# Kernel optimization log

Measured on AMD Instinct MI355X. Metric: run time of the kernel, lower is better.

## Reference

```python
import jax, jax.numpy as jnp
import numpy as np

DIM = 1024
NUM_HEADS = 16
HEAD_DIM = DIM // NUM_HEADS
EPS = 1e-5


def setup_inputs() -> dict:
    key = jax.random.key(0)
    ks = jax.random.split(key, 8)
    B, N = 4, 2048
    s = 0.02
    return {
        "x1": jax.random.normal(ks[0], (B, N, DIM), jnp.float32),
        "x2": jax.random.normal(ks[1], (B, N, DIM), jnp.float32),
        "wq": jax.random.normal(ks[2], (DIM, DIM), jnp.float32) * s,
        "bq": jnp.zeros((DIM,), jnp.float32),
        "wkv": jax.random.normal(ks[3], (DIM, 2 * DIM), jnp.float32) * s,
        "bkv": jnp.zeros((2 * DIM,), jnp.float32),
        "gamma_q": jnp.ones((HEAD_DIM,), jnp.float32),
        "beta_q": jnp.zeros((HEAD_DIM,), jnp.float32),
        "gamma_k": jnp.ones((HEAD_DIM,), jnp.float32),
        "beta_k": jnp.zeros((HEAD_DIM,), jnp.float32),
    }


def _layernorm(x, gamma, beta):
    m = jnp.mean(x, axis=-1, keepdims=True)
    v = jnp.mean(jnp.square(x - m), axis=-1, keepdims=True)
    return (x - m) * jax.lax.rsqrt(v + EPS) * gamma + beta


def reference(x1, x2, wq, bq, wkv, bkv, gamma_q, beta_q, gamma_k, beta_k):
    B, N, C = x1.shape
    H, D = NUM_HEADS, C // NUM_HEADS
    q = x1 @ wq + bq                      # [B,N,C]
    kv = x2 @ wkv + bkv                   # [B,N,2C]
    k, v = kv[..., :C], kv[..., C:]
    # [B,N,C] -> [B,H,N,D]
    q = q.reshape(B, N, H, D).transpose(0, 2, 1, 3)
    k = k.reshape(B, N, H, D).transpose(0, 2, 1, 3)
    v = v.reshape(B, N, H, D).transpose(0, 2, 1, 3)
    q = _layernorm(q, gamma_q, beta_q)
    k = _layernorm(k, gamma_k, beta_k)
    scale = 1.0 / jnp.sqrt(jnp.asarray(D, x1.dtype))
    scores = jnp.einsum("bhnd,bhmd->bhnm", q, k) * scale
    attn = jax.nn.softmax(scores, axis=-1)
    out = jnp.einsum("bhnm,bhmd->bhnd", attn, v)  # [B,H,N,D]
    return out.transpose(0, 2, 1, 3).reshape(B, N, C)
```

## Files before the change

### kernel.cpp

```cpp
#include <hip/hip_runtime.h>
#include <hip/hip_bf16.h>

#define NHEADS 16
#define HDIM 64
#define BATCH 4
#define SEQ 2048
#define CDIM 1024
#define ROWS (BATCH * SEQ)

typedef __attribute__((ext_vector_type(8))) short short8;
typedef __attribute__((ext_vector_type(4))) float f32x4;

__device__ inline short f2bf(float f) {
    unsigned int u = __builtin_bit_cast(unsigned int, f);
    unsigned int r = (u + 0x7fffu + ((u >> 16) & 1u)) >> 16;
    return (short)r;
}

__device__ __forceinline__ void gll16(const void* g, void* l) {
    __builtin_amdgcn_global_load_lds(
        (const __attribute__((address_space(1))) unsigned int*)g,
        (__attribute__((address_space(3))) unsigned int*)l, 16, 0, 0);
}

__global__ __launch_bounds__(256) void cvt_bf16(const float* __restrict__ src,
                                                short* __restrict__ dst, int n8) {
    int i = blockIdx.x * 256 + threadIdx.x;
    if (i < n8) {
        f32x4 a = ((const f32x4*)src)[i * 2];
        f32x4 b = ((const f32x4*)src)[i * 2 + 1];
        short8 o;
        o[0] = f2bf(a[0]); o[1] = f2bf(a[1]); o[2] = f2bf(a[2]); o[3] = f2bf(a[3]);
        o[4] = f2bf(b[0]); o[5] = f2bf(b[1]); o[6] = f2bf(b[2]); o[7] = f2bf(b[3]);
        ((short8*)dst)[i] = o;
    }
}

__global__ __launch_bounds__(256) void wtrans(const float* __restrict__ W,
                                              short* __restrict__ WT, int Nw) {
    __shared__ short T[64][72];
    const int t = threadIdx.x;
    const int n0 = blockIdx.x * 64, k0 = blockIdx.y * 64;
    const int kl = t >> 2, c4 = (t & 3) * 16;
    const float* src = W + (size_t)(k0 + kl) * Nw + n0 + c4;
    short8 s0, s1;
#pragma unroll
    for (int e = 0; e < 2; e++) {
        f32x4 u = *(const f32x4*)(src + e * 4);
        s0[e * 4 + 0] = f2bf(u[0]); s0[e * 4 + 1] = f2bf(u[1]);
        s0[e * 4 + 2] = f2bf(u[2]); s0[e * 4 + 3] = f2bf(u[3]);
        f32x4 v = *(const f32x4*)(src + 8 + e * 4);
        s1[e * 4 + 0] = f2bf(v[0]); s1[e * 4 + 1] = f2bf(v[1]);
        s1[e * 4 + 2] = f2bf(v[2]); s1[e * 4 + 3] = f2bf(v[3]);
    }
    *(short8*)&T[kl][c4] = s0;
    *(short8*)&T[kl][c4 + 8] = s1;
    __syncthreads();
#pragma unroll
    for (int pass = 0; pass < 2; pass++) {
        int n = (t >> 3) + pass * 32;
        short8 o;
#pragma unroll
        for (int e = 0; e < 8; e++) o[e] = T[(t & 7) * 8 + e][n];
        *(short8*)(WT + (size_t)(n0 + n) * 1024 + k0 + (t & 7) * 8) = o;
    }
}

__global__ __launch_bounds__(256) void gemm_q_ln(
    const short* __restrict__ A,
    const short* __restrict__ BT,
    const float* __restrict__ bias,
    const float* __restrict__ gamma,
    const float* __restrict__ beta,
    short* __restrict__ Out)
{
    __shared__ short As[128][32];
    __shared__ short Bs[128][32];

    const int tid = threadIdx.x;
    const int wave = tid >> 6, lane = tid & 63;
    const int wr = wave >> 1, wc = wave & 1;
    const int quad = lane >> 4, l15 = lane & 15;
    const int rblk = blockIdx.y, cblk = blockIdx.x;

    f32x4 acc[4][4];
#pragma unroll
    for (int i = 0; i < 4; i++)
#pragma unroll
        for (int j = 0; j < 4; j++) acc[i][j] = f32x4{0.f, 0.f, 0.f, 0.f};

    const int srow = wave * 32 + (lane >> 2);
    const int scol = (lane & 3) * 8;

    for (int k0 = 0; k0 < CDIM; k0 += 32) {
        __syncthreads();
#pragma unroll
        for (int c = 0; c < 2; c++) {
            gll16(A + (size_t)(rblk * 128 + srow + c * 16) * CDIM + k0 + scol,
                  &As[srow + c * 16][scol]);
            gll16(BT + (size_t)(cblk * 128 + srow + c * 16) * CDIM + k0 + scol,
                  &Bs[srow + c * 16][scol]);
        }
        __syncthreads();

        short8 af[4], bfr[4];
#pragma unroll
        for (int i = 0; i < 4; i++)
            af[i] = *(const short8*)&As[wr * 64 + i * 16 + l15][quad * 8];
#pragma unroll
        for (int j = 0; j < 4; j++)
            bfr[j] = *(const short8*)&Bs[wc * 64 + j * 16 + l15][quad * 8];
#pragma unroll
        for (int i = 0; i < 4; i++)
#pragma unroll
            for (int j = 0; j < 4; j++)
                acc[i][j] = __builtin_amdgcn_mfma_f32_16x16x32_bf16(af[i], bfr[j], acc[i][j], 0, 0, 0);
    }

    const int col0 = cblk * 128 + wc * 64;
    const int h = col0 >> 6;
    float bv[4], gv[4], btv[4];
#pragma unroll
    for (int j = 0; j < 4; j++) {
        int d = j * 16 + l15;
        bv[j] = bias[col0 + d];
        gv[j] = gamma[d];
        btv[j] = beta[d];
    }
#pragma unroll
    for (int i = 0; i < 4; i++) {
        int rowl = rblk * 128 + wr * 64 + i * 16 + quad * 4;
#pragma unroll
        for (int reg = 0; reg < 4; reg++) {
            float x[4], s = 0.f, s2 = 0.f;
#pragma unroll
            for (int j = 0; j < 4; j++) {
                x[j] = acc[i][j][reg] + bv[j];
                s += x[j];
                s2 += x[j] * x[j];
            }
#pragma unroll
            for (int m = 1; m < 16; m <<= 1) {
                s += __shfl_xor(s, m);
                s2 += __shfl_xor(s2, m);
            }
            float mean = s * (1.f / 64.f);
            float var = s2 * (1.f / 64.f) - mean * mean;
            float rstd = rsqrtf(var + 1e-5f);
            int r = rowl + reg;
            int b = r >> 11, n = r & (SEQ - 1);
            size_t base = (((size_t)b * NHEADS + h) * SEQ + n) * 64;
#pragma unroll
            for (int j = 0; j < 4; j++) {
                float y = ((x[j] - mean) * rstd * gv[j] + btv[j]) * 0.125f;
                Out[base + j * 16 + l15] = f2bf(y);
            }
        }
    }
}

__global__ __launch_bounds__(256) void gemm_kv(
    const short* __restrict__ A,
    const short* __restrict__ BT,
    const float* __restrict__ bias,
    const float* __restrict__ gamma,
    const float* __restrict__ beta,
    short* __restrict__ KOut,
    short* __restrict__ VT)
{
    __shared__ short As[128][32];
    __shared__ short Bs[128][32];
    __shared__ short Ts[4][64][68];

    const int tid = threadIdx.x;
    const int wave = tid >> 6, lane = tid & 63;
    const int wr = wave >> 1, wc = wave & 1;
    const int quad = lane >> 4, l15 = lane & 15;
    const int rblk = blockIdx.y, cblk = blockIdx.x;

    f32x4 acc[4][4];
#pragma unroll
    for (int i = 0; i < 4; i++)
#pragma unroll
        for (int j = 0; j < 4; j++) acc[i][j] = f32x4{0.f, 0.f, 0.f, 0.f};

    const int srow = wave * 32 + (lane >> 2);
    const int scol = (lane & 3) * 8;

    for (int k0 = 0; k0 < CDIM; k0 += 32) {
        __syncthreads();
#pragma unroll
        for (int c = 0; c < 2; c++) {
            gll16(A + (size_t)(rblk * 128 + srow + c * 16) * CDIM + k0 + scol,
                  &As[srow + c * 16][scol]);
            gll16(BT + (size_t)(cblk * 128 + srow + c * 16) * CDIM + k0 + scol,
                  &Bs[srow + c * 16][scol]);
        }
        __syncthreads();

        short8 af[4], bfr[4];
#pragma unroll
        for (int i = 0; i < 4; i++)
            af[i] = *(const short8*)&As[wr * 64 + i * 16 + l15][quad * 8];
#pragma unroll
        for (int j = 0; j < 4; j++)
            bfr[j] = *(const short8*)&Bs[wc * 64 + j * 16 + l15][quad * 8];
#pragma unroll
        for (int i = 0; i < 4; i++)
#pragma unroll
            for (int j = 0; j < 4; j++)
                acc[i][j] = __builtin_amdgcn_mfma_f32_16x16x32_bf16(af[i], bfr[j], acc[i][j], 0, 0, 0);
    }

    const int col0 = cblk * 128 + wc * 64;
    const int g = col0 >> 6;
    float bv[4];
#pragma unroll
    for (int j = 0; j < 4; j++) bv[j] = bias[col0 + j * 16 + l15];

    if (g < NHEADS) {
        const int h = g;
        float gv[4], btv[4];
#pragma unroll
        for (int j = 0; j < 4; j++) {
            int d = j * 16 + l15;
            gv[j] = gamma[d];
            btv[j] = beta[d];
        }
#pragma unroll
        for (int i = 0; i < 4; i++) {
            int rowl = rblk * 128 + wr * 64 + i * 16 + quad * 4;
#pragma unroll
            for (int reg = 0; reg < 4; reg++) {
                float x[4], s = 0.f, s2 = 0.f;
#pragma unroll
                for (int j = 0; j < 4; j++) {
                    x[j] = acc[i][j][reg] + bv[j];
                    s += x[j];
                    s2 += x[j] * x[j];
                }
#pragma unroll
                for (int m = 1; m < 16; m <<= 1) {
                    s += __shfl_xor(s, m);
                    s2 += __shfl_xor(s2, m);
                }
                float mean = s * (1.f / 64.f);
                float var = s2 * (1.f / 64.f) - mean * mean;
                float rstd = rsqrtf(var + 1e-5f);
                int r = rowl + reg;
                int b = r >> 11, n = r & (SEQ - 1);
                size_t base = (((size_t)b * NHEADS + h) * SEQ + n) * 64;
#pragma unroll
                for (int j = 0; j < 4; j++) {
                    float y = (x[j] - mean) * rstd * gv[j] + btv[j];
                    KOut[base + j * 16 + l15] = f2bf(y);
                }
            }
        }
    } else {
        const int h = g - NHEADS;
#pragma unroll
        for (int i = 0; i < 4; i++)
#pragma unroll
            for (int reg = 0; reg < 4; reg++)
#pragma unroll
                for (int j = 0; j < 4; j++)
                    Ts[wave][i * 16 + quad * 4 + reg][j * 16 + l15] =
                        f2bf(acc[i][j][reg] + bv[j]);
        const int r = rblk * 128 + wr * 64 + lane;
        const int b = r >> 11, n = r & (SEQ - 1);
        const size_t vtbase = (((size_t)b * NHEADS + h) * 64) * SEQ;
#pragma unroll
        for (int e8 = 0; e8 < 8; e8++) {
            short8 v = *(const short8*)&Ts[wave][lane][e8 * 8];
#pragma unroll
            for (int e = 0; e < 8; e++)
                VT[vtbase + (size_t)(e8 * 8 + e) * SEQ + n] = v[e];
        }
    }
}

__global__ __launch_bounds__(256) void attn_fa(
    const short* __restrict__ Q,
    const short* __restrict__ Kk,
    const short* __restrict__ VT,
    float* __restrict__ Out)
{
    __shared__ short Ks[128][72];
    __shared__ short Vt[64][136];
    __shared__ short Ps[4][16][136];

    const int tid = threadIdx.x;
    const int wave = tid >> 6, lane = tid & 63;
    const int quad = lane >> 4, l15 = lane & 15;
    const int bh = blockIdx.y;
    const int b = bh >> 4, h = bh & 15;
    const int qt = blockIdx.x;
    const size_t head_base = (size_t)bh * SEQ * 64;
    const size_t vt_base = (size_t)bh * 64 * SEQ;

    const int qrow = qt * 64 + wave * 16 + l15;
    const short8 qf0 = *(const short8*)(Q + head_base + (size_t)qrow * 64 + quad * 8);
    const short8 qf1 = *(const short8*)(Q + head_base + (size_t)qrow * 64 + 32 + quad * 8);

    short8 ones;
#pragma unroll
    for (int e = 0; e < 8; e++) ones[e] = (short)0x3F80;

    f32x4 o[4];
#pragma unroll
    for (int jd = 0; jd < 4; jd++) o[jd] = f32x4{0.f, 0.f, 0.f, 0.f};
    f32x4 osum = f32x4{0.f, 0.f, 0.f, 0.f};

    const int ks_key = tid >> 1, ks_c = (tid & 1) * 4;
    const int vt_d = tid >> 2, vt_c = (tid & 3) * 4;

    for (int kt = 0; kt < 16; kt++) {
        short8 kv[4], vv[4];
        const short* kg = Kk + head_base + (size_t)(kt * 128 + ks_key) * 64 + ks_c * 8;
        const short* vg = VT + vt_base + (size_t)vt_d * SEQ + kt * 128 + vt_c * 8;
#pragma unroll
        for (int i = 0; i < 4; i++) kv[i] = ((const short8*)kg)[i];
#pragma unroll
        for (int i = 0; i < 4; i++) vv[i] = ((const short8*)vg)[i];

        __syncthreads();
#pragma unroll
        for (int i = 0; i < 4; i++) *(short8*)&Ks[ks_key][(ks_c + i) * 8] = kv[i];
#pragma unroll
        for (int i = 0; i < 4; i++) *(short8*)&Vt[vt_d][(vt_c + i) * 8] = vv[i];
        __syncthreads();

        f32x4 s[8];
#pragma unroll
        for (int jk = 0; jk < 8; jk++) {
            short8 kf0 = *(const short8*)&Ks[jk * 16 + l15][quad * 8];
            short8 kf1 = *(const short8*)&Ks[jk * 16 + l15][32 + quad * 8];
            f32x4 z = f32x4{0.f, 0.f, 0.f, 0.f};
            z = __builtin_amdgcn_mfma_f32_16x16x32_bf16(qf0, kf0, z, 0, 0, 0);
            z = __builtin_amdgcn_mfma_f32_16x16x32_bf16(qf1, kf1, z, 0, 0, 0);
            s[jk] = z;
        }

#pragma unroll
        for (int jk = 0; jk < 8; jk++)
#pragma unroll
            for (int reg = 0; reg < 4; reg++)
                Ps[wave][quad * 4 + reg][jk * 16 + l15] = f2bf(__expf(s[jk][reg]));

        short8 pf[4];
#pragma unroll
        for (int seg = 0; seg < 4; seg++)
            pf[seg] = *(const short8*)&Ps[wave][l15][seg * 32 + quad * 8];

#pragma unroll
        for (int seg = 0; seg < 4; seg++)
            osum = __builtin_amdgcn_mfma_f32_16x16x32_bf16(pf[seg], ones, osum, 0, 0, 0);
#pragma unroll
        for (int seg = 0; seg < 4; seg++)
#pragma unroll
            for (int jd = 0; jd < 4; jd++) {
                short8 vf = *(const short8*)&Vt[jd * 16 + l15][seg * 32 + quad * 8];
                o[jd] = __builtin_amdgcn_mfma_f32_16x16x32_bf16(pf[seg], vf, o[jd], 0, 0, 0);
            }
    }

#pragma unroll
    for (int reg = 0; reg < 4; reg++) {
        float inv = 1.f / osum[reg];
        int r = qt * 64 + wave * 16 + quad * 4 + reg;
        size_t base = ((size_t)b * SEQ + r) * CDIM + h * 64;
#pragma unroll
        for (int jd = 0; jd < 4; jd++)
            Out[base + jd * 16 + l15] = o[jd][reg] * inv;
    }
}

extern "C" void kernel_launch(void* const* d_in, const int* in_sizes, int n_in,
                              void* d_out, int out_size, void* d_ws, size_t ws_size,
                              hipStream_t stream) {
    const float* x1 = (const float*)d_in[0];
    const float* x2 = (const float*)d_in[1];
    const float* wq = (const float*)d_in[2];
    const float* bq = (const float*)d_in[3];
    const float* wkv = (const float*)d_in[4];
    const float* bkv = (const float*)d_in[5];
    const float* gq = (const float*)d_in[6];
    const float* btq = (const float*)d_in[7];
    const float* gk = (const float*)d_in[8];
    const float* btk = (const float*)d_in[9];
    float* out = (float*)d_out;

    short* a1 = (short*)d_ws;
    short* a2 = a1 + (size_t)ROWS * CDIM;
    short* wqT = a2 + (size_t)ROWS * CDIM;
    short* wkvT = wqT + (size_t)CDIM * CDIM;
    short* qln = wkvT + (size_t)2 * CDIM * CDIM;
    short* kln = qln + (size_t)ROWS * CDIM;
    short* vt = kln + (size_t)ROWS * CDIM;

    const int n8 = ROWS * CDIM / 8;
    cvt_bf16<<<dim3(n8 / 256), 256, 0, stream>>>(x1, a1, n8);
    cvt_bf16<<<dim3(n8 / 256), 256, 0, stream>>>(x2, a2, n8);
    wtrans<<<dim3(16, 16), 256, 0, stream>>>(wq, wqT, CDIM);
    wtrans<<<dim3(32, 16), 256, 0, stream>>>(wkv, wkvT, 2 * CDIM);

    gemm_q_ln<<<dim3(8, 64), 256, 0, stream>>>(a1, wqT, bq, gq, btq, qln);
    gemm_kv<<<dim3(16, 64), 256, 0, stream>>>(a2, wkvT, bkv, gk, btk, kln, vt);
    attn_fa<<<dim3(32, 64), 256, 0, stream>>>(qln, kln, vt, out);
}
```

Measured before the change: 357.1 us.

## Split attention keys across waves with register-direct K/V and cross-wave reduction

```diff
diff --git a/kernel.cpp b/kernel.cpp
--- a/kernel.cpp
+++ b/kernel.cpp
@@ -7,9 +7,11 @@
 #define SEQ 2048
 #define CDIM 1024
 #define ROWS (BATCH * SEQ)
+#define QSCALE (0.125f * 1.44269504088896f)
 
 typedef __attribute__((ext_vector_type(8))) short short8;
 typedef __attribute__((ext_vector_type(4))) float f32x4;
+typedef __attribute__((ext_vector_type(4))) unsigned int u32x4;
 
 __device__ inline short f2bf(float f) {
     unsigned int u = __builtin_bit_cast(unsigned int, f);
@@ -21,6 +23,11 @@
     __builtin_amdgcn_global_load_lds(
         (const __attribute__((address_space(1))) unsigned int*)g,
         (__attribute__((address_space(3))) unsigned int*)l, 16, 0, 0);
+}
+
+__device__ __forceinline__ unsigned int pack_bf2(float a, float b) {
+    return __builtin_amdgcn_perm(__builtin_bit_cast(unsigned int, b),
+                                 __builtin_bit_cast(unsigned int, a), 0x07060302u);
 }
 
 __global__ __launch_bounds__(256) void cvt_bf16(const float* __restrict__ src,
@@ -152,7 +159,7 @@
             size_t base = (((size_t)b * NHEADS + h) * SEQ + n) * 64;
 #pragma unroll
             for (int j = 0; j < 4; j++) {
-                float y = ((x[j] - mean) * rstd * gv[j] + btv[j]) * 0.125f;
+                float y = ((x[j] - mean) * rstd * gv[j] + btv[j]) * QSCALE;
                 Out[base + j * 16 + l15] = f2bf(y);
             }
         }
@@ -286,93 +293,147 @@
     const short* __restrict__ VT,
     float* __restrict__ Out)
 {
-    __shared__ short Ks[128][72];
-    __shared__ short Vt[64][136];
-    __shared__ short Ps[4][16][136];
+    __shared__ float smem[12544];
 
     const int tid = threadIdx.x;
-    const int wave = tid >> 6, lane = tid & 63;
-    const int quad = lane >> 4, l15 = lane & 15;
+    const int w = tid >> 6, lane = tid & 63;
+    const int q = lane >> 4, l15 = lane & 15;
     const int bh = blockIdx.y;
     const int b = bh >> 4, h = bh & 15;
     const int qt = blockIdx.x;
-    const size_t head_base = (size_t)bh * SEQ * 64;
-    const size_t vt_base = (size_t)bh * 64 * SEQ;
-
-    const int qrow = qt * 64 + wave * 16 + l15;
-    const short8 qf0 = *(const short8*)(Q + head_base + (size_t)qrow * 64 + quad * 8);
-    const short8 qf1 = *(const short8*)(Q + head_base + (size_t)qrow * 64 + 32 + quad * 8);
+    const size_t hb = (size_t)bh * SEQ * 64;
+    const size_t vb = (size_t)bh * 64 * SEQ;
+
+    short8 qf[4][2];
+#pragma unroll
+    for (int qc = 0; qc < 4; qc++)
+#pragma unroll
+        for (int dh = 0; dh < 2; dh++)
+            qf[qc][dh] = *(const short8*)(Q + hb +
+                (size_t)(qt * 64 + qc * 16 + l15) * 64 + dh * 32 + q * 8);
 
     short8 ones;
 #pragma unroll
     for (int e = 0; e < 8; e++) ones[e] = (short)0x3F80;
 
-    f32x4 o[4];
-#pragma unroll
-    for (int jd = 0; jd < 4; jd++) o[jd] = f32x4{0.f, 0.f, 0.f, 0.f};
-    f32x4 osum = f32x4{0.f, 0.f, 0.f, 0.f};
-
-    const int ks_key = tid >> 1, ks_c = (tid & 1) * 4;
-    const int vt_d = tid >> 2, vt_c = (tid & 3) * 4;
-
-    for (int kt = 0; kt < 16; kt++) {
-        short8 kv[4], vv[4];
-        const short* kg = Kk + head_base + (size_t)(kt * 128 + ks_key) * 64 + ks_c * 8;
-        const short* vg = VT + vt_base + (size_t)vt_d * SEQ + kt * 128 + vt_c * 8;
-#pragma unroll
-        for (int i = 0; i < 4; i++) kv[i] = ((const short8*)kg)[i];
-#pragma unroll
-        for (int i = 0; i < 4; i++) vv[i] = ((const short8*)vg)[i];
-
-        __syncthreads();
-#pragma unroll
-        for (int i = 0; i < 4; i++) *(short8*)&Ks[ks_key][(ks_c + i) * 8] = kv[i];
-#pragma unroll
-        for (int i = 0; i < 4; i++) *(short8*)&Vt[vt_d][(vt_c + i) * 8] = vv[i];
-        __syncthreads();
-
-        f32x4 s[8];
-#pragma unroll
-        for (int jk = 0; jk < 8; jk++) {
-            short8 kf0 = *(const short8*)&Ks[jk * 16 + l15][quad * 8];
-            short8 kf1 = *(const short8*)&Ks[jk * 16 + l15][32 + quad * 8];
-            f32x4 z = f32x4{0.f, 0.f, 0.f, 0.f};
-            z = __builtin_amdgcn_mfma_f32_16x16x32_bf16(qf0, kf0, z, 0, 0, 0);
-            z = __builtin_amdgcn_mfma_f32_16x16x32_bf16(qf1, kf1, z, 0, 0, 0);
-            s[jk] = z;
-        }
-
-#pragma unroll
-        for (int jk = 0; jk < 8; jk++)
-#pragma unroll
-            for (int reg = 0; reg < 4; reg++)
-                Ps[wave][quad * 4 + reg][jk * 16 + l15] = f2bf(__expf(s[jk][reg]));
+    f32x4 o[4][4];
+#pragma unroll
+    for (int jd = 0; jd < 4; jd++)
+#pragma unroll
+        for (int qc = 0; qc < 4; qc++) o[jd][qc] = f32x4{0.f, 0.f, 0.f, 0.f};
+    f32x4 osum[4];
+#pragma unroll
+    for (int qc = 0; qc < 4; qc++) osum[qc] = f32x4{0.f, 0.f, 0.f, 0.f};
+
+    unsigned int* Pd = (unsigned int*)smem + w * 1280;
+
+    const short* kbase = Kk + hb + (size_t)(w * 32 + l15) * 64 + q * 8;
+    const short* vbase = VT + vb + (size_t)l15 * SEQ + w * 32 + q * 8;
+
+    short8 kf[2][2];
+#pragma unroll
+    for (int kt = 0; kt < 2; kt++)
+#pragma unroll
+        for (int dh = 0; dh < 2; dh++)
+            kf[kt][dh] = *(const short8*)(kbase + (size_t)(kt * 16) * 64 + dh * 32);
+
+    for (int kti = 0; kti < 16; kti++) {
+        short8 vf[4];
+#pragma unroll
+        for (int jd = 0; jd < 4; jd++)
+            vf[jd] = *(const short8*)(vbase + (size_t)(jd * 16) * SEQ + kti * 128);
+
+        f32x4 s[2][4];
+#pragma unroll
+        for (int kt = 0; kt < 2; kt++)
+#pragma unroll
+            for (int qc = 0; qc < 4; qc++) {
+                f32x4 z = f32x4{0.f, 0.f, 0.f, 0.f};
+                z = __builtin_amdgcn_mfma_f32_16x16x32_bf16(kf[kt][0], qf[qc][0], z, 0, 0, 0);
+                z = __builtin_amdgcn_mfma_f32_16x16x32_bf16(kf[kt][1], qf[qc][1], z, 0, 0, 0);
+                s[kt][qc] = z;
+            }
+
+        int knx = kti + 1 < 16 ? kti + 1 : 15;
+        short8 kn[2][2];
+#pragma unroll
+        for (int kt = 0; kt < 2; kt++)
+#pragma unroll
+            for (int dh = 0; dh < 2; dh++)
+                kn[kt][dh] = *(const short8*)(kbase +
+                    (size_t)(knx * 128 + kt * 16) * 64 + dh * 32);
+
+#pragma unroll
+        for (int kt = 0; kt < 2; kt++)
+#pragma unroll
+            for (int qc = 0; qc < 4; qc++) {
+                float p0 = __builtin_amdgcn_exp2f(s[kt][qc][0]);
+                float p1 = __builtin_amdgcn_exp2f(s[kt][qc][1]);
+                float p2 = __builtin_amdgcn_exp2f(s[kt][qc][2]);
+                float p3 = __builtin_amdgcn_exp2f(s[kt][qc][3]);
+                unsigned int d0 = pack_bf2(p0, p1);
+                unsigned int d1 = pack_bf2(p2, p3);
+                unsigned int* p = &Pd[(qc * 16 + l15) * 20 + kt * 8 + 2 * q];
+                p[0] = d0;
+                p[1] = d1;
+            }
 
         short8 pf[4];
 #pragma unroll
-        for (int seg = 0; seg < 4; seg++)
-            pf[seg] = *(const short8*)&Ps[wave][l15][seg * 32 + quad * 8];
-
-#pragma unroll
-        for (int seg = 0; seg < 4; seg++)
-            osum = __builtin_amdgcn_mfma_f32_16x16x32_bf16(pf[seg], ones, osum, 0, 0, 0);
-#pragma unroll
-        for (int seg = 0; seg < 4; seg++)
-#pragma unroll
-            for (int jd = 0; jd < 4; jd++) {
-                short8 vf = *(const short8*)&Vt[jd * 16 + l15][seg * 32 + quad * 8];
-                o[jd] = __builtin_amdgcn_mfma_f32_16x16x32_bf16(pf[seg], vf, o[jd], 0, 0, 0);
-            }
-    }
-
-#pragma unroll
-    for (int reg = 0; reg < 4; reg++) {
-        float inv = 1.f / osum[reg];
-        int r = qt * 64 + wave * 16 + quad * 4 + reg;
-        size_t base = ((size_t)b * SEQ + r) * CDIM + h * 64;
+        for (int qc = 0; qc < 4; qc++) {
+            u32x4 pr = *(const u32x4*)&Pd[(qc * 16 + l15) * 20 + 4 * q];
+            pf[qc] = __builtin_bit_cast(short8, pr);
+        }
+
+#pragma unroll
+        for (int qc = 0; qc < 4; qc++)
+            osum[qc] = __builtin_amdgcn_mfma_f32_16x16x32_bf16(ones, pf[qc], osum[qc], 0, 0, 0);
 #pragma unroll
         for (int jd = 0; jd < 4; jd++)
-            Out[base + jd * 16 + l15] = o[jd][reg] * inv;
+#pragma unroll
+            for (int qc = 0; qc < 4; qc++)
+                o[jd][qc] = __builtin_amdgcn_mfma_f32_16x16x32_bf16(vf[jd], pf[qc], o[jd][qc], 0, 0, 0);
+
+#pragma unroll
+        for (int kt = 0; kt < 2; kt++)
+#pragma unroll
+            for (int dh = 0; dh < 2; dh++) kf[kt][dh] = kn[kt][dh];
+    }
+
+    __syncthreads();
+    float* Ored = smem;
+    float* Lred = smem + 12288;
+#pragma unroll
+    for (int jd = 0; jd < 4; jd++) {
+        if (jd == w) continue;
+        int sl = w - (w > jd ? 1 : 0);
+#pragma unroll
+        for (int qc = 0; qc < 4; qc++)
+            *(f32x4*)&Ored[(((jd * 3 + sl) * 4 + qc) * 64 + lane) * 4] = o[jd][qc];
+    }
+    if (q == 0) {
+#pragma unroll
+        for (int qc = 0; qc < 4; qc++)
+            Lred[w * 64 + qc * 16 + l15] = osum[qc][0];
+    }
+    __syncthreads();
+
+#pragma unroll
+    for (int sl = 0; sl < 3; sl++)
+#pragma unroll
+        for (int qc = 0; qc < 4; qc++) {
+            f32x4 t = *(const f32x4*)&Ored[(((w * 3 + sl) * 4 + qc) * 64 + lane) * 4];
+            o[w][qc] += t;
+        }
+
+#pragma unroll
+    for (int qc = 0; qc < 4; qc++) {
+        float l = Lred[qc * 16 + l15] + Lred[64 + qc * 16 + l15] +
+                  Lred[128 + qc * 16 + l15] + Lred[192 + qc * 16 + l15];
+        float inv = 1.f / l;
+        f32x4 r = o[w][qc] * inv;
+        int row = qt * 64 + qc * 16 + l15;
+        *(f32x4*)(Out + ((size_t)b * SEQ + row) * CDIM + h * 64 + w * 16 + 4 * q) = r;
     }
 }
 
```

Result: slower. 396.5 us (+11.0%).
